# Kernel optimization log

Measured on AMD Instinct MI355X. Metric: run time of the kernel, lower is better.

The kernel has to match this reference:

```python
import jax, jax.numpy as jnp
import numpy as np

N = 100000   # nodes
E = 1600000  # edges (before self loops)
F = 64       # num_features
H = 64       # hidden_channels
C = 10       # num_classes
G = 128      # graphs in batch
NEG_SLOPE = 0.2


def setup_inputs() -> dict:
    key = jax.random.key(0)
    ks = jax.random.split(key, 16)
    x = jax.random.normal(ks[0], (N, F), dtype=jnp.float32)
    edge_index = jax.random.randint(ks[1], (2, E), 0, N, dtype=jnp.int64)
    batch = jnp.sort(jax.random.randint(ks[2], (N,), 0, G, dtype=jnp.int64))
    def glorot(k, shape):
        fan = shape[0] + shape[-1]
        return jax.random.uniform(k, shape, jnp.float32, -1.0, 1.0) * np.sqrt(6.0 / fan)
    return {
        "x": x, "edge_index": edge_index, "batch": batch,
        # GATConv 1 (F -> H)
        "W1": glorot(ks[3], (F, H)), "as1": glorot(ks[4], (H,)), "ad1": glorot(ks[5], (H,)), "b1": jnp.zeros((H,), jnp.float32),
        # GATConv 2 (H -> H)
        "W2": glorot(ks[6], (H, H)), "as2": glorot(ks[7], (H,)), "ad2": glorot(ks[8], (H,)), "b2": jnp.zeros((H,), jnp.float32),
        # MLP head
        "mw1": glorot(ks[9], (H, H)), "mb1": jnp.zeros((H,), jnp.float32),
        "mw2": glorot(ks[10], (H, C)), "mb2": jnp.zeros((C,), jnp.float32),
    }


def gat_conv(x, src, dst, W, a_s, a_d, b):
    # x: [N, Fin] -> h: [N, Fout]
    h = x @ W
    # per-node attention halves, gathered per edge (heads=1)
    al_s = h @ a_s   # [N]
    al_d = h @ a_d   # [N]
    e = jax.nn.leaky_relu(al_s[src] + al_d[dst], NEG_SLOPE)  # [E']
    # segment softmax over incoming edges of each destination node
    m = jax.ops.segment_max(e, dst, num_segments=N)
    ex = jnp.exp(e - m[dst])
    denom = jax.ops.segment_sum(ex, dst, num_segments=N)
    alpha = ex / denom[dst]                                   # [E']
    # weighted scatter-add of source features
    out = jax.ops.segment_sum(alpha[:, None] * h[src], dst, num_segments=N)
    return out + b


def reference(x, edge_index, batch, W1, as1, ad1, b1, W2, as2, ad2, b2, mw1, mb1, mw2, mb2):
    # add self loops (PyG GATConv default)
    loop = jnp.arange(N, dtype=edge_index.dtype)
    src = jnp.concatenate([edge_index[0], loop])
    dst = jnp.concatenate([edge_index[1], loop])

    h = gat_conv(x, src, dst, W1, as1, ad1, b1)
    h = jax.nn.elu(h)  # dropout p=0.5 is identity in eval mode
    h = gat_conv(h, src, dst, W2, as2, ad2, b2)
    h = jax.nn.elu(h)

    h = jax.nn.relu(h @ mw1 + mb1) @ mw2 + mb2   # MLP [N, C]
    return jax.ops.segment_sum(h, batch, num_segments=G)  # global_add_pool [G, C]
```

## Files before the change

### kernel.cpp

```cpp
#include <hip/hip_runtime.h>
#include <hip/hip_bf16.h>
#include <math.h>

#define SHIFT 20.0f
#define T_PER 32
#define TILE (256 * T_PER)
#define BCAP 5248
#define LS_T 1024
#define MS_LDS 36864

typedef __bf16 bf16x8 __attribute__((ext_vector_type(8)));
typedef float  f32x4  __attribute__((ext_vector_type(4)));

__device__ __forceinline__ unsigned f2bf(float f) {
    unsigned u = __float_as_uint(f);
    return (u + 0x7fffu + ((u >> 16) & 1u)) >> 16;
}

__global__ void setup_kernel(float* __restrict__ Pz, int nPz,
                             const float* __restrict__ W1,
                             const float* __restrict__ as1, const float* __restrict__ ad1,
                             const float* __restrict__ W2,
                             const float* __restrict__ as2, const float* __restrict__ ad2,
                             const float* __restrict__ mw1,
                             uint4* __restrict__ Wf1, uint4* __restrict__ Wf2,
                             uint4* __restrict__ mwf)
{
    int t = threadIdx.x;
    if (blockIdx.x == 0) {
        for (int i = t; i < nPz; i += 256) Pz[i] = 0.f;
        return;
    }
    __shared__ float wasad[256];
    {
        int k = t & 63;
        const float* W  = (t < 128) ? W1 : W2;
        const float* av = (t < 64) ? as1 : (t < 128) ? ad1 : (t < 192) ? as2 : ad2;
        float s = 0.f;
        for (int n = 0; n < 64; n++) s = fmaf(W[k * 64 + n], av[n], s);
        wasad[t] = s;
    }
    __syncthreads();

    for (int idx = t; idx < 1792; idx += 256) {
        const float* W; const float* wv; uint4* dst; int rem;
        if (idx < 640)       { rem = idx;        W = W1;  wv = &wasad[0];   dst = Wf1; }
        else if (idx < 1280) { rem = idx - 640;  W = W2;  wv = &wasad[128]; dst = Wf2; }
        else                 { rem = idx - 1280; W = mw1; wv = nullptr;     dst = mwf; }
        int pair = rem >> 6, l = rem & 63;
        int tt = pair >> 1, s = pair & 1;
        int kb = s * 32 + (l >> 4) * 8;
        unsigned d[4];
        if (tt < 4) {
            int n = tt * 16 + (l & 15);
            #pragma unroll
            for (int j = 0; j < 4; j++)
                d[j] = f2bf(W[(kb + 2 * j) * 64 + n]) |
                       (f2bf(W[(kb + 2 * j + 1) * 64 + n]) << 16);
        } else {
            int n0 = l & 15;
            #pragma unroll
            for (int j = 0; j < 4; j++) {
                float v0 = (n0 == 0) ? wv[kb + 2 * j]     : (n0 == 1) ? wv[64 + kb + 2 * j]     : 0.f;
                float v1 = (n0 == 0) ? wv[kb + 2 * j + 1] : (n0 == 1) ? wv[64 + kb + 2 * j + 1] : 0.f;
                d[j] = f2bf(v0) | (f2bf(v1) << 16);
            }
        }
        dst[pair * 64 + l] = make_uint4(d[0], d[1], d[2], d[3]);
    }
}

__device__ __forceinline__ void multisplit_body(
    unsigned char* ldsraw, const int* __restrict__ esrc, const int* __restrict__ edst,
    unsigned short* __restrict__ stab, unsigned* __restrict__ pairbuf,
    int nE, int tot, int K2, int TW, int tile)
{
    int* lcur   = (int*)ldsraw;
    unsigned* seg = (unsigned*)(lcur + 512);
    int t = threadIdx.x;
    int base = tile * TILE;
    int cnt_tile = min(TILE, tot - base);

    for (int i = t; i < 512; i += 256) lcur[i] = 0;
    __syncthreads();

    #pragma unroll
    for (int i = 0; i < T_PER; i++) {
        int e = base + t + i * 256;
        if (e < tot) {
            int d = (e < nE) ? edst[e] : (e - nE);
            atomicAdd(&lcur[d >> 8], 1);
        }
    }
    __syncthreads();

    if (t < 64) {
        int c[8]; int s = 0;
        #pragma unroll
        for (int k = 0; k < 8; k++) { c[k] = lcur[t * 8 + k]; s += c[k]; }
        int run = s;
        #pragma unroll
        for (int off = 1; off < 64; off <<= 1) {
            int u = __shfl_up(run, off);
            if (t >= off) run += u;
        }
        int st = run - s;
        #pragma unroll
        for (int k = 0; k < 8; k++) {
            int slot = t * 8 + k;
            lcur[slot] = st;
            if (slot <= K2) stab[(size_t)tile * TW + slot] = (unsigned short)st;
            st += c[k];
        }
    }
    __syncthreads();

    #pragma unroll
    for (int i = 0; i < T_PER; i++) {
        int e = base + t + i * 256;
        if (e < tot) {
            int s = (e < nE) ? esrc[e] : (e - nE);
            int d = (e < nE) ? edst[e] : (e - nE);
            int p = atomicAdd(&lcur[d >> 8], 1);
            seg[p] = ((unsigned)s << 8) | (unsigned)(d & 255);
        }
    }
    __syncthreads();

    for (int j = t; j < cnt_tile; j += 256)
        pairbuf[base + j] = seg[j];
}

__device__ __forceinline__ void gemm_body(
    unsigned char* lds, const void* __restrict__ Xv, int x_is_bf16,
    const uint4* __restrict__ Wf, __hip_bfloat16* __restrict__ Hout,
    float* __restrict__ als, float* __restrict__ ald, int nN, int b0)
{
    int t = threadIdx.x, lane = t & 63, wv = t >> 6;

    uint4 wf[10];
    #pragma unroll
    for (int p = 0; p < 10; p++) wf[p] = Wf[p * 64 + lane];

    if (x_is_bf16) {
        const uint4* X4 = (const uint4*)Xv;
        int limit = nN * 8;
        #pragma unroll
        for (int k = 0; k < 8; k++) {
            int dst = t + k * 256;
            int idx = b0 * 8 + dst;
            if (idx < limit) {
                int r = dst >> 3, c = dst & 7;
                *(uint4*)(lds + r * 144 + c * 16) = X4[idx];
            }
        }
    } else {
        const float4* Xf = (const float4*)Xv;
        int limit = nN * 16;
        #pragma unroll
        for (int k = 0; k < 16; k++) {
            int dst = t + k * 256;
            int idx = b0 * 16 + dst;
            if (idx < limit) {
                float4 v = Xf[idx];
                uint2 r2;
                r2.x = f2bf(v.x) | (f2bf(v.y) << 16);
                r2.y = f2bf(v.z) | (f2bf(v.w) << 16);
                int r = dst >> 4, c = dst & 15;
                *(uint2*)(lds + r * 144 + c * 8) = r2;
            }
        }
    }
    __syncthreads();

    f32x4 acc[4][5] = {};
    int rbase = wv * 64;
    #pragma unroll
    for (int s = 0; s < 2; s++) {
        #pragma unroll
        for (int rf = 0; rf < 4; rf++) {
            const uint4 av = *(const uint4*)(lds + (rbase + rf * 16 + (lane & 15)) * 144
                                                 + s * 64 + (lane >> 4) * 16);
            bf16x8 a = __builtin_bit_cast(bf16x8, av);
            #pragma unroll
            for (int tt = 0; tt < 5; tt++) {
                bf16x8 b = __builtin_bit_cast(bf16x8, wf[tt * 2 + s]);
                acc[rf][tt] = __builtin_amdgcn_mfma_f32_16x16x32_bf16(a, b, acc[rf][tt], 0, 0, 0);
            }
        }
    }

    int q = lane >> 4, c = lane & 15;
    #pragma unroll
    for (int rf = 0; rf < 4; rf++) {
        #pragma unroll
        for (int r = 0; r < 4; r++) {
            int n = b0 + rbase + rf * 16 + q * 4 + r;
            if (n < nN) {
                #pragma unroll
                for (int tt = 0; tt < 4; tt++)
                    Hout[(size_t)n * 64 + tt * 16 + c] = __float2bfloat16(acc[rf][tt][r]);
                if (c == 0)      als[n] = acc[rf][4][r];
                else if (c == 1) ald[n] = acc[rf][4][r];
            }
        }
    }
}

__global__ __launch_bounds__(256) void ms_gemm_kernel(
    const int* __restrict__ esrc, const int* __restrict__ edst,
    unsigned short* __restrict__ stab, unsigned* __restrict__ pairbuf,
    int nE, int nN, int K2, int TW, int nTiles,
    const void* __restrict__ Xv, const uint4* __restrict__ Wf,
    __hip_bfloat16* __restrict__ Hout,
    float* __restrict__ als, float* __restrict__ ald)
{
    __shared__ __align__(16) unsigned char lds[MS_LDS];
    if (blockIdx.x < nTiles) {
        multisplit_body(lds, esrc, edst, stab, pairbuf, nE, nE + nN, K2, TW, blockIdx.x);
    } else {
        gemm_body(lds, Xv, 0, Wf, Hout, als, ald, nN, (blockIdx.x - nTiles) * 256);
    }
}

__global__ __launch_bounds__(256) void gemm_att_mfma(
    const void* __restrict__ Xv, int x_is_bf16,
    const uint4* __restrict__ Wf,
    __hip_bfloat16* __restrict__ Hout,
    float* __restrict__ als, float* __restrict__ ald, int nN)
{
    __shared__ __align__(16) unsigned char lds[256 * 144];
    gemm_body(lds, Xv, x_is_bf16, Wf, Hout, als, ald, nN, blockIdx.x * 256);
}

__global__ __launch_bounds__(LS_T) void local_scatter_kernel(
    const unsigned* __restrict__ pairbuf, const unsigned short* __restrict__ stab,
    int2* __restrict__ rp2, int* __restrict__ csr_src,
    int nN, int K2, int TW, int nTiles)
{
    __shared__ unsigned seg[BCAP];
    __shared__ int lh[256];
    __shared__ int cur[256];
    __shared__ int tstart[256], toff[256], tlen[256];
    __shared__ int ltot;
    int b = blockIdx.x;
    int t = threadIdx.x;
    int wv = t >> 6, lane = t & 63;
    int d0 = b * 256;
    int nd = min(256, nN - d0);
    int lo = b * BCAP;

    if (t < 256) lh[t] = 0;
    if (t < 64) {
        int ln[4], gs[4]; int s = 0;
        #pragma unroll
        for (int k = 0; k < 4; k++) {
            int tile = t * 4 + k;
            int l = 0, g = 0;
            if (tile < nTiles) {
                int st = stab[(size_t)tile * TW + b];
                int en = stab[(size_t)tile * TW + b + 1];
                l = en - st;
                g = tile * TILE + st;
            }
            ln[k] = l; gs[k] = g; s += l;
        }
        int run = s;
        #pragma unroll
        for (int off = 1; off < 64; off <<= 1) {
            int u = __shfl_up(run, off);
            if (t >= off) run += u;
        }
        int off0 = run - s;
        #pragma unroll
        for (int k = 0; k < 4; k++) {
            int tile = t * 4 + k;
            if (tile < nTiles) { toff[tile] = off0; tstart[tile] = gs[k]; tlen[tile] = ln[k]; }
            off0 += ln[k];
        }
        if (t == 63) ltot = run;
    }
    __syncthreads();
    int len = min(ltot, BCAP);

    for (int tile = wv; tile < nTiles; tile += LS_T / 64) {
        int l = tlen[tile], o = toff[tile], g = tstart[tile];
        for (int j = lane; j < l; j += 64)
            if (o + j < BCAP) seg[o + j] = pairbuf[g + j];
    }
    __syncthreads();
    for (int j = t; j < len; j += LS_T) atomicAdd(&lh[seg[j] & 255u], 1);
    __syncthreads();

    if (t < 64) {
        int b4 = t * 4;
        int c0 = lh[b4], c1 = lh[b4 + 1], c2 = lh[b4 + 2], c3 = lh[b4 + 3];
        int tot4 = c0 + c1 + c2 + c3;
        int run = tot4;
        #pragma unroll
        for (int off = 1; off < 64; off <<= 1) {
            int u = __shfl_up(run, off);
            if (t >= off) run += u;
        }
        int e0 = lo + run - tot4;
        int e1 = e0 + c0, e2 = e1 + c1, e3 = e2 + c2;
        cur[b4] = e0; cur[b4 + 1] = e1; cur[b4 + 2] = e2; cur[b4 + 3] = e3;
        if (b4 < nd)     rp2[d0 + b4]     = make_int2(e0, c0);
        if (b4 + 1 < nd) rp2[d0 + b4 + 1] = make_int2(e1, c1);
        if (b4 + 2 < nd) rp2[d0 + b4 + 2] = make_int2(e2, c2);
        if (b4 + 3 < nd) rp2[d0 + b4 + 3] = make_int2(e3, c3);
    }
    __syncthreads();

    for (int j = t; j < len; j += LS_T) {
        unsigned w = seg[j];
        int pos = atomicAdd(&cur[w & 255u], 1);
        csr_src[pos] = (int)(w >> 8);
    }
}

__global__ __launch_bounds__(256) void pull_kernel(
    const int* __restrict__ csr_src, const int2* __restrict__ rp2,
    const unsigned* __restrict__ Hu,
    const float* __restrict__ als, const float* __restrict__ ald,
    const float* __restrict__ bias,
    __hip_bfloat162* __restrict__ out2, int dlo, int dhi)
{
    int lane = threadIdx.x & 63;
    int half = lane >> 5;
    int fl = lane & 31;
    int wid  = (blockIdx.x * blockDim.x + threadIdx.x) >> 6;
    int nw   = (gridDim.x * blockDim.x) >> 6;
    float2 bl2 = ((const float2*)bias)[fl];

    for (int d = dlo + wid; d < dhi; d += nw) {
        int2 rp = rp2[d];
        int s0 = rp.x, m = rp.y;
        float aldd = ald[d];
        float aclo = 0.f, achi = 0.f, den = 0.f;

        for (int base = 0; base < m; base += 64) {
            int j = base + lane;
            bool v = (j < m);
            int sl = v ? csr_src[s0 + j] : 0;
            float ex = 0.f;
            if (v) {
                float sc = als[sl] + aldd;
                sc = (sc > 0.f) ? sc : 0.2f * sc;
                ex = __expf(sc - SHIFT);
            }
            float es = ex;
            #pragma unroll
            for (int off = 32; off > 0; off >>= 1) es += __shfl_xor(es, off);
            den += es;

            int mm = min(64, m - base);
            int sA = __shfl(sl, half), sB = __shfl(sl, 2 + half);
            float eA = __shfl(ex, half), eB = __shfl(ex, 2 + half);
            unsigned dA = Hu[((unsigned)sA << 5) | fl];
            unsigned dB = Hu[((unsigned)sB << 5) | fl];
            for (int i2 = 0; i2 < mm; i2 += 4) {
                int i4 = (i2 + 4) & 63;
                int   sA2 = __shfl(sl, i4 + half);
                int   sB2 = __shfl(sl, i4 + 2 + half);
                float eA2 = __shfl(ex, i4 + half);
                float eB2 = __shfl(ex, i4 + 2 + half);
                unsigned dA2 = Hu[((unsigned)sA2 << 5) | fl];
                unsigned dB2 = Hu[((unsigned)sB2 << 5) | fl];
                aclo = fmaf(eA, __uint_as_float(dA << 16), aclo);
                achi = fmaf(eA, __uint_as_float(dA & 0xffff0000u), achi);
                aclo = fmaf(eB, __uint_as_float(dB << 16), aclo);
                achi = fmaf(eB, __uint_as_float(dB & 0xffff0000u), achi);
                sA = sA2; sB = sB2; eA = eA2; eB = eB2; dA = dA2; dB = dB2;
            }
        }
        aclo += __shfl_xor(aclo, 32);
        achi += __shfl_xor(achi, 32);
        float v0 = aclo / den + bl2.x;
        float v1 = achi / den + bl2.y;
        v0 = (v0 > 0.f) ? v0 : expm1f(v0);
        v1 = (v1 > 0.f) ? v1 : expm1f(v1);
        if (half == 0) {
            __hip_bfloat162 pk;
            pk.x = __float2bfloat16(v0);
            pk.y = __float2bfloat16(v1);
            out2[((unsigned)d << 5) | fl] = pk;
        }
    }
}

__global__ __launch_bounds__(256) void mlp_pool_mfma(
    const uint4* __restrict__ Hin,
    const uint4* __restrict__ mwf, const float* __restrict__ mb1,
    const int* __restrict__ batch,
    float* __restrict__ P, float* __restrict__ Pcnt, int nN)
{
    __shared__ __align__(16) unsigned char lds[256 * 144];
    int t = threadIdx.x, lane = t & 63, wv = t >> 6;
    int b0 = blockIdx.x * 256;

    uint4 wf[8];
    #pragma unroll
    for (int p = 0; p < 8; p++) wf[p] = mwf[p * 64 + lane];

    int limit = nN * 8;
    #pragma unroll
    for (int k = 0; k < 8; k++) {
        int dst = t + k * 256;
        int idx = b0 * 8 + dst;
        if (idx < limit) {
            int r = dst >> 3, c = dst & 7;
            *(uint4*)(lds + r * 144 + c * 16) = Hin[idx];
        }
    }
    __syncthreads();

    f32x4 acc[4][4] = {};
    int rbase = wv * 64;
    #pragma unroll
    for (int s = 0; s < 2; s++) {
        #pragma unroll
        for (int rf = 0; rf < 4; rf++) {
            const uint4 av = *(const uint4*)(lds + (rbase + rf * 16 + (lane & 15)) * 144
                                                 + s * 64 + (lane >> 4) * 16);
            bf16x8 a = __builtin_bit_cast(bf16x8, av);
            #pragma unroll
            for (int tt = 0; tt < 4; tt++) {
                bf16x8 b = __builtin_bit_cast(bf16x8, wf[tt * 2 + s]);
                acc[rf][tt] = __builtin_amdgcn_mfma_f32_16x16x32_bf16(a, b, acc[rf][tt], 0, 0, 0);
            }
        }
    }

    int q = lane >> 4, c = lane & 15;
    float bl0 = mb1[c], bl1 = mb1[16 + c], bl2 = mb1[32 + c], bl3 = mb1[48 + c];
    float r0 = 0.f, r1 = 0.f, r2 = 0.f, r3 = 0.f, ccnt = 0.f;
    int gcur = -1;
    #pragma unroll
    for (int rf = 0; rf < 4; rf++) {
        #pragma unroll
        for (int r = 0; r < 4; r++) {
            int n = b0 + rbase + rf * 16 + q * 4 + r;
            if (n < nN) {
                int g = batch[n];
                if (g != gcur) {
                    if (gcur >= 0) {
                        atomicAdd(&P[(size_t)gcur * 64 + c],      r0);
                        atomicAdd(&P[(size_t)gcur * 64 + 16 + c], r1);
                        atomicAdd(&P[(size_t)gcur * 64 + 32 + c], r2);
                        atomicAdd(&P[(size_t)gcur * 64 + 48 + c], r3);
                        if (c == 0) atomicAdd(&Pcnt[gcur], ccnt);
                    }
                    gcur = g; r0 = r1 = r2 = r3 = 0.f; ccnt = 0.f;
                }
                r0 += fmaxf(acc[rf][0][r] + bl0, 0.f);
                r1 += fmaxf(acc[rf][1][r] + bl1, 0.f);
                r2 += fmaxf(acc[rf][2][r] + bl2, 0.f);
                r3 += fmaxf(acc[rf][3][r] + bl3, 0.f);
                ccnt += 1.f;
            }
        }
    }
    if (gcur >= 0) {
        atomicAdd(&P[(size_t)gcur * 64 + c],      r0);
        atomicAdd(&P[(size_t)gcur * 64 + 16 + c], r1);
        atomicAdd(&P[(size_t)gcur * 64 + 32 + c], r2);
        atomicAdd(&P[(size_t)gcur * 64 + 48 + c], r3);
        if (c == 0) atomicAdd(&Pcnt[gcur], ccnt);
    }
}

__global__ void head_out_kernel(const float* __restrict__ P,
                                const float* __restrict__ Pcnt,
                                const float* __restrict__ mw2,
                                const float* __restrict__ mb2,
                                float* __restrict__ out, int nOut)
{
    int t = blockIdx.x * blockDim.x + threadIdx.x;
    if (t >= nOut) return;
    int g = t / 10, j = t % 10;
    float s = mb2[j] * Pcnt[g];
    const float* pr = P + (size_t)g * 64;
    #pragma unroll
    for (int k = 0; k < 64; k++) s = fmaf(pr[k], mw2[k * 10 + j], s);
    out[t] = s;
}

extern "C" void kernel_launch(void* const* d_in, const int* in_sizes, int n_in,
                              void* d_out, int out_size, void* d_ws, size_t ws_size,
                              hipStream_t stream)
{
    const float* x   = (const float*)d_in[0];
    const int*  eidx = (const int*)d_in[1];
    const int* batch = (const int*)d_in[2];
    const float* W1  = (const float*)d_in[3];
    const float* as1 = (const float*)d_in[4];
    const float* ad1 = (const float*)d_in[5];
    const float* b1  = (const float*)d_in[6];
    const float* W2  = (const float*)d_in[7];
    const float* as2 = (const float*)d_in[8];
    const float* ad2 = (const float*)d_in[9];
    const float* b2  = (const float*)d_in[10];
    const float* mw1 = (const float*)d_in[11];
    const float* mb1 = (const float*)d_in[12];
    const float* mw2 = (const float*)d_in[13];
    const float* mb2 = (const float*)d_in[14];
    float* out = (float*)d_out;

    int nN = in_sizes[0] / 64;
    int nE = in_sizes[1] / 2;
    int tot = nE + nN;
    int K2 = (nN + 255) >> 8;
    int TW = K2 + 1;
    int G  = out_size / 10;
    const int* esrc = eidx;
    const int* edst = eidx + nE;

    int nTiles = (tot + TILE - 1) / TILE;
    int nT256 = (nN + 255) / 256;
    int nHalf = nN / 2;

    float* ws = (float*)d_ws;
    size_t NF = (size_t)nN * 64;
    size_t capTot = (size_t)K2 * BCAP;
    size_t pbTot  = (size_t)nTiles * TILE;
    float* bufA   = ws;
    float* bufB   = ws + NF;
    float* als    = ws + 2 * NF;
    float* ald    = als + nN;
    int2* rp2     = (int2*)(ald + nN);
    int* csr_src  = (int*)(rp2 + nN);
    unsigned short* stab = (unsigned short*)(csr_src + capTot);
    float* P      = (float*)(((uintptr_t)(stab + (size_t)nTiles * TW) + 63)
                             & ~(uintptr_t)63);
    float* Pcnt   = P + (size_t)G * 64;
    uintptr_t wb  = ((uintptr_t)(Pcnt + G) + 255) & ~(uintptr_t)255;
    uint4* Wf1    = (uint4*)wb;
    uint4* Wf2    = Wf1 + 640;
    uint4* mwf    = Wf2 + 640;
    unsigned* pairbuf = (unsigned*)bufA;
    __hip_bfloat16* hbf = (__hip_bfloat16*)bufB;
    (void)pbTot;

    dim3 blk(256);

    setup_kernel<<<2, blk, 0, stream>>>(P, G * 64 + G,
                                        W1, as1, ad1, W2, as2, ad2, mw1,
                                        Wf1, Wf2, mwf);
    ms_gemm_kernel<<<nTiles + nT256, blk, 0, stream>>>(
        esrc, edst, stab, pairbuf, nE, nN, K2, TW, nTiles,
        x, Wf1, hbf, als, ald);
    local_scatter_kernel<<<K2, dim3(LS_T), 0, stream>>>(pairbuf, stab, rp2,
                                                        csr_src, nN, K2, TW,
                                                        nTiles);

    pull_kernel<<<2048, blk, 0, stream>>>(csr_src, rp2, (const unsigned*)hbf,
                                          als, ald, b1,
                                          (__hip_bfloat162*)bufA, 0, nHalf);
    pull_kernel<<<2048, blk, 0, stream>>>(csr_src, rp2, (const unsigned*)hbf,
                                          als, ald, b1,
                                          (__hip_bfloat162*)bufA, nHalf, nN);
    gemm_att_mfma<<<nT256, blk, 0, stream>>>(bufA, 1, Wf2, hbf, als, ald, nN);
    pull_kernel<<<2048, blk, 0, stream>>>(csr_src, rp2, (const unsigned*)hbf,
                                          als, ald, b2,
                                          (__hip_bfloat162*)bufA, 0, nHalf);
    pull_kernel<<<2048, blk, 0, stream>>>(csr_src, rp2, (const unsigned*)hbf,
                                          als, ald, b2,
                                          (__hip_bfloat162*)bufA, nHalf, nN);

    mlp_pool_mfma<<<nT256, blk, 0, stream>>>((const uint4*)bufA, mwf, mb1,
                                             batch, P, Pcnt, nN);
    head_out_kernel<<<(out_size + 255) / 256, blk, 0, stream>>>(P, Pcnt, mw2,
                                                                mb2, out, out_size);
}
```

Measured before the change: 296.0 us.

## Split multisplit into standalone 1024-thread kernel with smaller tiles; merge pull launches

Turns the edge multisplit into its own kernel using 1024-thread blocks and 4096-edge tiles. This roughly doubles the tile count, so more blocks can run across the CUs. The first-layer GEMM now runs as a separate launch instead of sharing a fused grid with the multisplit. Local scatter's per-tile tables grow to 512 entries to cover the larger tile count. Each layer's two half-range pull launches become a single full-range launch, which saves launch overhead but loses any locality the half split gave and the overlap the fused grid allowed.

```diff
diff --git a/kernel.cpp b/kernel.cpp
--- a/kernel.cpp
+++ b/kernel.cpp
@@ -3,11 +3,11 @@
 #include <math.h>
 
 #define SHIFT 20.0f
-#define T_PER 32
-#define TILE (256 * T_PER)
+#define MS_T 1024
+#define T_PER 4
+#define TILE (MS_T * T_PER)
 #define BCAP 5248
 #define LS_T 1024
-#define MS_LDS 36864
 
 typedef __bf16 bf16x8 __attribute__((ext_vector_type(8)));
 typedef float  f32x4  __attribute__((ext_vector_type(4)));
@@ -70,23 +70,25 @@
     }
 }
 
-__device__ __forceinline__ void multisplit_body(
-    unsigned char* ldsraw, const int* __restrict__ esrc, const int* __restrict__ edst,
+__global__ __launch_bounds__(MS_T) void multisplit_kernel(
+    const int* __restrict__ esrc, const int* __restrict__ edst,
     unsigned short* __restrict__ stab, unsigned* __restrict__ pairbuf,
-    int nE, int tot, int K2, int TW, int tile)
-{
-    int* lcur   = (int*)ldsraw;
-    unsigned* seg = (unsigned*)(lcur + 512);
+    int nE, int nN, int K2, int TW)
+{
+    __shared__ int lcur[512];
+    __shared__ unsigned seg[TILE];
     int t = threadIdx.x;
+    int tile = blockIdx.x;
+    int tot = nE + nN;
     int base = tile * TILE;
     int cnt_tile = min(TILE, tot - base);
 
-    for (int i = t; i < 512; i += 256) lcur[i] = 0;
+    if (t < 512) lcur[t] = 0;
     __syncthreads();
 
     #pragma unroll
     for (int i = 0; i < T_PER; i++) {
-        int e = base + t + i * 256;
+        int e = base + t + i * MS_T;
         if (e < tot) {
             int d = (e < nE) ? edst[e] : (e - nE);
             atomicAdd(&lcur[d >> 8], 1);
@@ -117,7 +119,7 @@
 
     #pragma unroll
     for (int i = 0; i < T_PER; i++) {
-        int e = base + t + i * 256;
+        int e = base + t + i * MS_T;
         if (e < tot) {
             int s = (e < nE) ? esrc[e] : (e - nE);
             int d = (e < nE) ? edst[e] : (e - nE);
@@ -127,16 +129,19 @@
     }
     __syncthreads();
 
-    for (int j = t; j < cnt_tile; j += 256)
+    for (int j = t; j < cnt_tile; j += MS_T)
         pairbuf[base + j] = seg[j];
 }
 
-__device__ __forceinline__ void gemm_body(
-    unsigned char* lds, const void* __restrict__ Xv, int x_is_bf16,
-    const uint4* __restrict__ Wf, __hip_bfloat16* __restrict__ Hout,
-    float* __restrict__ als, float* __restrict__ ald, int nN, int b0)
-{
+__global__ __launch_bounds__(256) void gemm_att_mfma(
+    const void* __restrict__ Xv, int x_is_bf16,
+    const uint4* __restrict__ Wf,
+    __hip_bfloat16* __restrict__ Hout,
+    float* __restrict__ als, float* __restrict__ ald, int nN)
+{
+    __shared__ __align__(16) unsigned char lds[256 * 144];
     int t = threadIdx.x, lane = t & 63, wv = t >> 6;
+    int b0 = blockIdx.x * 256;
 
     uint4 wf[10];
     #pragma unroll
@@ -207,32 +212,6 @@
     }
 }
 
-__global__ __launch_bounds__(256) void ms_gemm_kernel(
-    const int* __restrict__ esrc, const int* __restrict__ edst,
-    unsigned short* __restrict__ stab, unsigned* __restrict__ pairbuf,
-    int nE, int nN, int K2, int TW, int nTiles,
-    const void* __restrict__ Xv, const uint4* __restrict__ Wf,
-    __hip_bfloat16* __restrict__ Hout,
-    float* __restrict__ als, float* __restrict__ ald)
-{
-    __shared__ __align__(16) unsigned char lds[MS_LDS];
-    if (blockIdx.x < nTiles) {
-        multisplit_body(lds, esrc, edst, stab, pairbuf, nE, nE + nN, K2, TW, blockIdx.x);
-    } else {
-        gemm_body(lds, Xv, 0, Wf, Hout, als, ald, nN, (blockIdx.x - nTiles) * 256);
-    }
-}
-
-__global__ __launch_bounds__(256) void gemm_att_mfma(
-    const void* __restrict__ Xv, int x_is_bf16,
-    const uint4* __restrict__ Wf,
-    __hip_bfloat16* __restrict__ Hout,
-    float* __restrict__ als, float* __restrict__ ald, int nN)
-{
-    __shared__ __align__(16) unsigned char lds[256 * 144];
-    gemm_body(lds, Xv, x_is_bf16, Wf, Hout, als, ald, nN, blockIdx.x * 256);
-}
-
 __global__ __launch_bounds__(LS_T) void local_scatter_kernel(
     const unsigned* __restrict__ pairbuf, const unsigned short* __restrict__ stab,
     int2* __restrict__ rp2, int* __restrict__ csr_src,
@@ -241,7 +220,7 @@
     __shared__ unsigned seg[BCAP];
     __shared__ int lh[256];
     __shared__ int cur[256];
-    __shared__ int tstart[256], toff[256], tlen[256];
+    __shared__ int tstart[512], toff[512], tlen[512];
     __shared__ int ltot;
     int b = blockIdx.x;
     int t = threadIdx.x;
@@ -252,10 +231,10 @@
 
     if (t < 256) lh[t] = 0;
     if (t < 64) {
-        int ln[4], gs[4]; int s = 0;
-        #pragma unroll
-        for (int k = 0; k < 4; k++) {
-            int tile = t * 4 + k;
+        int ln[8], gs[8]; int s = 0;
+        #pragma unroll
+        for (int k = 0; k < 8; k++) {
+            int tile = t * 8 + k;
             int l = 0, g = 0;
             if (tile < nTiles) {
                 int st = stab[(size_t)tile * TW + b];
@@ -273,8 +252,8 @@
         }
         int off0 = run - s;
         #pragma unroll
-        for (int k = 0; k < 4; k++) {
-            int tile = t * 4 + k;
+        for (int k = 0; k < 8; k++) {
+            int tile = t * 8 + k;
             if (tile < nTiles) { toff[tile] = off0; tstart[tile] = gs[k]; tlen[tile] = ln[k]; }
             off0 += ln[k];
         }
@@ -324,7 +303,7 @@
     const unsigned* __restrict__ Hu,
     const float* __restrict__ als, const float* __restrict__ ald,
     const float* __restrict__ bias,
-    __hip_bfloat162* __restrict__ out2, int dlo, int dhi)
+    __hip_bfloat162* __restrict__ out2, int nN)
 {
     int lane = threadIdx.x & 63;
     int half = lane >> 5;
@@ -333,7 +312,7 @@
     int nw   = (gridDim.x * blockDim.x) >> 6;
     float2 bl2 = ((const float2*)bias)[fl];
 
-    for (int d = dlo + wid; d < dhi; d += nw) {
+    for (int d = wid; d < nN; d += nw) {
         int2 rp = rp2[d];
         int s0 = rp.x, m = rp.y;
         float aldd = ald[d];
@@ -518,12 +497,10 @@
 
     int nTiles = (tot + TILE - 1) / TILE;
     int nT256 = (nN + 255) / 256;
-    int nHalf = nN / 2;
 
     float* ws = (float*)d_ws;
     size_t NF = (size_t)nN * 64;
     size_t capTot = (size_t)K2 * BCAP;
-    size_t pbTot  = (size_t)nTiles * TILE;
     float* bufA   = ws;
     float* bufB   = ws + NF;
     float* als    = ws + 2 * NF;
@@ -540,33 +517,26 @@
     uint4* mwf    = Wf2 + 640;
     unsigned* pairbuf = (unsigned*)bufA;
     __hip_bfloat16* hbf = (__hip_bfloat16*)bufB;
-    (void)pbTot;
 
     dim3 blk(256);
 
     setup_kernel<<<2, blk, 0, stream>>>(P, G * 64 + G,
                                         W1, as1, ad1, W2, as2, ad2, mw1,
                                         Wf1, Wf2, mwf);
-    ms_gemm_kernel<<<nTiles + nT256, blk, 0, stream>>>(
-        esrc, edst, stab, pairbuf, nE, nN, K2, TW, nTiles,
-        x, Wf1, hbf, als, ald);
+    multisplit_kernel<<<nTiles, dim3(MS_T), 0, stream>>>(
+        esrc, edst, stab, pairbuf, nE, nN, K2, TW);
+    gemm_att_mfma<<<nT256, blk, 0, stream>>>(x, 0, Wf1, hbf, als, ald, nN);
     local_scatter_kernel<<<K2, dim3(LS_T), 0, stream>>>(pairbuf, stab, rp2,
                                                         csr_src, nN, K2, TW,
                                                         nTiles);
 
     pull_kernel<<<2048, blk, 0, stream>>>(csr_src, rp2, (const unsigned*)hbf,
                                           als, ald, b1,
-                                          (__hip_bfloat162*)bufA, 0, nHalf);
-    pull_kernel<<<2048, blk, 0, stream>>>(csr_src, rp2, (const unsigned*)hbf,
-                                          als, ald, b1,
-                                          (__hip_bfloat162*)bufA, nHalf, nN);
+                                          (__hip_bfloat162*)bufA, nN);
     gemm_att_mfma<<<nT256, blk, 0, stream>>>(bufA, 1, Wf2, hbf, als, ald, nN);
     pull_kernel<<<2048, blk, 0, stream>>>(csr_src, rp2, (const unsigned*)hbf,
                                           als, ald, b2,
-                                          (__hip_bfloat162*)bufA, 0, nHalf);
-    pull_kernel<<<2048, blk, 0, stream>>>(csr_src, rp2, (const unsigned*)hbf,
-                                          als, ald, b2,
-                                          (__hip_bfloat162*)bufA, nHalf, nN);
+                                          (__hip_bfloat162*)bufA, nN);
 
     mlp_pool_mfma<<<nT256, blk, 0, stream>>>((const uint4*)bufA, mwf, mb1,
                                              batch, P, Pcnt, nN);
```

Result: faster. 289.8 us (-2.1%).
